# Kernel optimization log

Measured on AMD Instinct MI355X. Metric: run time of the kernel, lower is better.

Reference implementation:

```python
import jax, jax.numpy as jnp
import numpy as np

B, C, L = 2048, 9605, 8
ALPHA = 0.5        # self.alpha
ALPHA1 = 0.05      # margin
ALPHA2 = 2.0       # asymmetric scale when violated
ALPHA3 = 5.0       # logistic sharpness
ALPHA_OTHER = 0.3  # floor on top-k threshold
TOPK = 16          # x_sorted[15] -> 16th largest


def setup_inputs() -> dict:
    key = jax.random.key(0)
    k1, k2, k3, k4 = jax.random.split(key, 4)
    x = jax.random.normal(k1, (B, C), dtype=jnp.float32)
    # each class assigned to one of 5*L slots; slots < L are whitelist groups,
    # the rest are 'other' classes (like total_indices in the torch code)
    gid = jax.random.randint(k4, (C,), 0, 5 * L)
    gid = gid.at[:L].set(jnp.arange(L))  # guarantee every group is non-empty
    group_mask = gid[None, :] == jnp.arange(L)[:, None]  # [L, C] bool
    # sparse multi-label binarized targets (~14 positives/sample)
    y = (jax.random.uniform(k2, (B, C)) < 0.0015).astype(jnp.float32)
    y_neg = (jax.random.uniform(k3, (B, C)) < 0.0015).astype(jnp.float32)
    return {"x": x, "y": y, "y_neg": y_neg, "group_mask": group_mask}


def _rank_loss(x1, x2):
    # our_rank_loss: sigmoid(alpha3*(x2-x1+margin)), scaled by alpha2 when violated
    d = x2 - x1 + ALPHA1
    s = jax.nn.sigmoid(ALPHA3 * d)
    return jnp.where(d > 0, ALPHA2 * s, s)


def reference(x, y, y_neg, group_mask):
    xs = jax.nn.sigmoid(x)  # [B, C]
    # top_k_thres = max(16th-largest sigmoid score, alpha_other)
    thres = jnp.maximum(jax.lax.top_k(xs, TOPK)[0][:, TOPK - 1], ALPHA_OTHER)  # [B]
    maskf = group_mask.astype(xs.dtype)  # [L, C]
    neg_inf = jnp.array(-jnp.inf, xs.dtype)
    # per-sample max score inside each whitelist group: [B, L]
    group_max = jnp.max(jnp.where(group_mask[None, :, :], xs[:, None, :], neg_inf), axis=-1)
    # find_gt_whitelist: group is 'hit' if any positive target inside it
    gt = (y @ maskf.T) > 0        # [B, L]
    gt_neg = (y_neg @ maskf.T) > 0  # [B, L]
    has_gt = jnp.any(gt, axis=-1)    # [B]; False <=> sentinel len(all_labels)
    has_neg = jnp.any(gt_neg, axis=-1)
    # ---- case B: sample hits at least one whitelist group ----
    rl_correct = _rank_loss(group_max, thres[:, None])    # gt groups above thres
    rl_incorrect = _rank_loss(thres[:, None], group_max)  # non-gt groups below thres
    caseB = jnp.sum(jnp.where(gt, rl_correct, rl_incorrect), axis=-1)  # [B]
    # ---- case A: no whitelist group hit ----
    union = jnp.any(group_mask, axis=0)  # [C] union of all whitelist classes
    union_max = jnp.max(jnp.where(union[None, :], xs, neg_inf), axis=-1)  # [B]
    neg_max = jnp.max(jnp.where(gt_neg, group_max, neg_inf), axis=-1)
    neg_score = jnp.where(has_neg, neg_max, jnp.zeros((), xs.dtype))  # torch starts at 0
    caseA = (1.0 - ALPHA) * _rank_loss(thres, union_max) + ALPHA * _rank_loss(thres, neg_score)
    loss_rank_all = jnp.where(has_gt, caseB, caseA)  # [B]
    return jnp.mean(loss_rank_all)
```

## Files before the change

### kernel.cpp

```cpp
#include <hip/hip_runtime.h>
#include <math.h>

constexpr int B_ = 2048;
constexpr int C_ = 9605;
constexpr int L_ = 8;
constexpr int TOPK_ = 16;
constexpr int CAP_ = 512;
constexpr int NSLOT_ = 8;
constexpr float T0_ = 2.0f;
constexpr int QW_ = 2404;

__device__ __forceinline__ float sigm(float v) { return 1.0f / (1.0f + expf(-v)); }

__device__ __forceinline__ float rank_loss(float x1, float x2) {
  float d = x2 - x1 + 0.05f;
  float s = 1.0f / (1.0f + expf(-5.0f * d));
  return (d > 0.0f) ? 2.0f * s : s;
}

__device__ __forceinline__ unsigned int fkey(float v) {
  unsigned int u = __float_as_uint(v);
  return u ^ ((u & 0x80000000u) ? 0xFFFFFFFFu : 0x80000000u);
}
__device__ __forceinline__ float fkeyinv(unsigned int k) {
  unsigned int u = (k & 0x80000000u) ? (k ^ 0x80000000u) : ~k;
  return __uint_as_float(u);
}

__global__ void build_code_kernel(const int* __restrict__ mask,
                                  unsigned char* __restrict__ code) {
  int c = blockIdx.x * 256 + threadIdx.x;
  if (c >= C_) return;
  unsigned char cd = 0xFF;
#pragma unroll
  for (int l = L_ - 1; l >= 0; --l)
    if (mask[l * C_ + c] != 0) cd = (unsigned char)l;
  code[c] = cd;
}

__global__ void pack_code_kernel(const unsigned char* __restrict__ code,
                                 unsigned int* __restrict__ codeq) {
  int k = blockIdx.x * 256 + threadIdx.x;
  int r = blockIdx.y;
  if (k >= QW_) return;
  unsigned int v = 0u;
#pragma unroll
  for (int e = 0; e < 4; ++e) {
    int c = r + 4 * k + e;
    unsigned int byte = (c < C_) ? (unsigned int)code[c] : 0xFFu;
    v |= byte << (8 * e);
  }
  codeq[r * QW_ + k] = v;
}

__global__ void __launch_bounds__(256) row_loss_kernel(
    const float* __restrict__ x, const float* __restrict__ y,
    const float* __restrict__ yn, const unsigned char* __restrict__ code,
    const unsigned int* __restrict__ codeq, float* __restrict__ loss) {
  __shared__ float cand[CAP_];
  __shared__ int cand_cnt;
  __shared__ int s_of;
  __shared__ float wgm[4][L_];
  __shared__ unsigned int wgt[4], wgn[4];
  __shared__ float s_x16;
  __shared__ int s_red;

  const int t = threadIdx.x;
  const int b = blockIdx.x;
  const float* xr = x + (size_t)b * C_;
  const float* yr = y + (size_t)b * C_;
  const float* ynr = yn + (size_t)b * C_;

  if (t == 0) { cand_cnt = 0; s_of = 0; }

  float gm[L_];
#pragma unroll
  for (int l = 0; l < L_; ++l) gm[l] = -INFINITY;
  unsigned int gtb = 0u, gnb = 0u;
  float cnd[NSLOT_];
  int cc = 0;
#pragma unroll
  for (int k = 0; k < NSLOT_; ++k) cnd[k] = -INFINITY;

  auto proc = [&](float xv, float yv, float nv, int cd) {
#pragma unroll
    for (int l = 0; l < L_; ++l)
      if (cd == l) gm[l] = fmaxf(gm[l], xv);
    unsigned int mb = (cd < L_) ? (1u << (cd & 7)) : 0u;
    gtb |= (yv > 0.0f) ? mb : 0u;
    gnb |= (nv > 0.0f) ? mb : 0u;
    int cci = (xv > T0_) ? cc : NSLOT_;
#pragma unroll
    for (int k = 0; k < NSLOT_; ++k)
      if (cci == k) cnd[k] = xv;
    cc += (xv > T0_) ? 1 : 0;
  };

  const int r = b & 3;
  const int lead = (4 - r) & 3;
  const int n4 = (C_ - lead) >> 2;
  const float4* x4 = reinterpret_cast<const float4*>(x) + (((size_t)b * C_ + lead) >> 2);
  const float4* y4 = reinterpret_cast<const float4*>(y) + (((size_t)b * C_ + lead) >> 2);
  const float4* v4 = reinterpret_cast<const float4*>(yn) + (((size_t)b * C_ + lead) >> 2);
  const unsigned int* cq = codeq + lead * QW_;

  for (int k = t; k < n4; k += 256) {
    float4 xv = x4[k];
    float4 yv = y4[k];
    float4 nv = v4[k];
    unsigned int cqk = cq[k];
    proc(xv.x, yv.x, nv.x, (int)(cqk & 0xFF));
    proc(xv.y, yv.y, nv.y, (int)((cqk >> 8) & 0xFF));
    proc(xv.z, yv.z, nv.z, (int)((cqk >> 16) & 0xFF));
    proc(xv.w, yv.w, nv.w, (int)((cqk >> 24) & 0xFF));
  }
  if (t < lead) proc(xr[t], yr[t], ynr[t], (int)code[t]);
  const int tstart = lead + (n4 << 2);
  if (t >= 4 && t < 4 + (C_ - tstart)) {
    int c = tstart + (t - 4);
    proc(xr[c], yr[c], ynr[c], (int)code[c]);
  }

#pragma unroll
  for (int off = 32; off > 0; off >>= 1) {
#pragma unroll
    for (int l = 0; l < L_; ++l) gm[l] = fmaxf(gm[l], __shfl_xor(gm[l], off, 64));
    gtb |= (unsigned int)__shfl_xor((int)gtb, off, 64);
    gnb |= (unsigned int)__shfl_xor((int)gnb, off, 64);
  }

  __syncthreads();

  int nw = (cc < NSLOT_) ? cc : NSLOT_;
  if (nw > 0) {
    int pos = atomicAdd(&cand_cnt, nw);
#pragma unroll
    for (int k = 0; k < NSLOT_; ++k)
      if (k < nw && pos + k < CAP_) cand[pos + k] = cnd[k];
  }
  if (cc > NSLOT_) atomicOr(&s_of, 1);

  if ((t & 63) == 0) {
    int w = t >> 6;
#pragma unroll
    for (int l = 0; l < L_; ++l) wgm[w][l] = gm[l];
    wgt[w] = gtb;
    wgn[w] = gnb;
  }
  __syncthreads();

  const int cnt = cand_cnt;
  const bool mainp = (cnt >= TOPK_) && (cnt <= CAP_) && (s_of == 0);
  if (mainp) {
    if (t < 64) {
      unsigned int ku[CAP_ / 64];
#pragma unroll
      for (int k = 0; k < CAP_ / 64; ++k) {
        int idx = t + (k << 6);
        ku[k] = (idx < cnt) ? fkey(cand[idx]) : 0u;
      }
      unsigned int lo = 0u, hi = 0xFFFFFFFFu;
      for (int it = 0; it < 32 && lo < hi; ++it) {
        unsigned int mid = lo + ((hi - lo) >> 1) + 1u;
        int c16 = 0;
#pragma unroll
        for (int k = 0; k < CAP_ / 64; ++k) c16 += (ku[k] >= mid) ? 1 : 0;
#pragma unroll
        for (int off = 32; off > 0; off >>= 1) c16 += __shfl_xor(c16, off, 64);
        if (c16 >= TOPK_) lo = mid; else hi = mid - 1u;
      }
      if (t == 0) s_x16 = fkeyinv(lo);
    }
  } else {
    unsigned int lo = 0u, hi = 0xFFFFFFFFu;
    for (int it = 0; it < 32; ++it) {
      if (lo >= hi) break;
      unsigned int mid = lo + ((hi - lo) >> 1) + 1u;
      if (t == 0) s_red = 0;
      __syncthreads();
      int cl = 0;
      for (int c = t; c < C_; c += 256) cl += (fkey(xr[c]) >= mid) ? 1 : 0;
      atomicAdd(&s_red, cl);
      __syncthreads();
      int total = s_red;
      __syncthreads();
      if (total >= TOPK_) lo = mid; else hi = mid - 1u;
    }
    if (t == 0) s_x16 = fkeyinv(lo);
  }
  __syncthreads();

  if (t == 0) {
    float thres = fmaxf(sigm(s_x16), 0.3f);
    unsigned int gtbf = wgt[0] | wgt[1] | wgt[2] | wgt[3];
    unsigned int gnbf = wgn[0] | wgn[1] | wgn[2] | wgn[3];
    float caseB = 0.0f, unio = -INFINITY, negmax = -INFINITY;
#pragma unroll
    for (int l = 0; l < L_; ++l) {
      float gx = fmaxf(fmaxf(wgm[0][l], wgm[1][l]), fmaxf(wgm[2][l], wgm[3][l]));
      float g = sigm(gx);
      unio = fmaxf(unio, g);
      caseB += ((gtbf >> l) & 1u) ? rank_loss(g, thres) : rank_loss(thres, g);
      if ((gnbf >> l) & 1u) negmax = fmaxf(negmax, g);
    }
    float negscore = (gnbf != 0u) ? negmax : 0.0f;
    float caseA = 0.5f * rank_loss(thres, unio) + 0.5f * rank_loss(thres, negscore);
    loss[b] = (gtbf != 0u) ? caseB : caseA;
  }
}

__global__ void mean_kernel(const float* __restrict__ loss, float* __restrict__ out) {
  const int t = threadIdx.x;
  float s = 0.0f;
  for (int i = t; i < B_; i += 256) s += loss[i];
#pragma unroll
  for (int off = 32; off > 0; off >>= 1) s += __shfl_xor(s, off, 64);
  __shared__ float part[4];
  if ((t & 63) == 0) part[t >> 6] = s;
  __syncthreads();
  if (t == 0) out[0] = (part[0] + part[1] + part[2] + part[3]) * (1.0f / (float)B_);
}

extern "C" void kernel_launch(void* const* d_in, const int* in_sizes, int n_in,
                              void* d_out, int out_size, void* d_ws, size_t ws_size,
                              hipStream_t stream) {
  const float* x = (const float*)d_in[0];
  const float* y = (const float*)d_in[1];
  const float* yn = (const float*)d_in[2];
  const int* mask = (const int*)d_in[3];

  float* loss = (float*)d_ws;
  unsigned char* code = (unsigned char*)d_ws + 8192;
  unsigned int* codeq = (unsigned int*)((char*)d_ws + 8192 + 9612);

  hipLaunchKernelGGL(build_code_kernel, dim3((C_ + 255) / 256), dim3(256), 0, stream,
                     mask, code);
  hipLaunchKernelGGL(pack_code_kernel, dim3((QW_ + 255) / 256, 4), dim3(256), 0, stream,
                     code, codeq);
  hipLaunchKernelGGL(row_loss_kernel, dim3(B_), dim3(256), 0, stream,
                     x, y, yn, code, codeq, loss);
  hipLaunchKernelGGL(mean_kernel, dim3(1), dim3(256), 0, stream,
                     loss, (float*)d_out);
}
```

Before: 262.0 us.

## Split sparse target scanning into separate grid-wide kernel with atomic group bits

Moves the scan of y and y_neg out of the per-row kernel into a dedicated grid-stride kernel that streams both arrays and atomically ORs group bits only for rare positive entries. The row kernel now reads just x and the packed codes, with unrolled float4 loads and a direct shared-memory atomic append for candidates in place of per-thread slot registers. The aim is to cut per-row work and register pressure and raise memory parallelism. The cost is an extra memset, an extra kernel launch and global atomics, and total traffic over y and y_neg is unchanged.

New measurement: 262.1 us. Within noise of the previous version (+0.0%).

```diff
diff --git a/kernel.cpp b/kernel.cpp
--- a/kernel.cpp
+++ b/kernel.cpp
@@ -6,9 +6,9 @@
 constexpr int L_ = 8;
 constexpr int TOPK_ = 16;
 constexpr int CAP_ = 512;
-constexpr int NSLOT_ = 8;
 constexpr float T0_ = 2.0f;
 constexpr int QW_ = 2404;
+constexpr int NQ_ = (B_ * C_) / 4;
 
 __device__ __forceinline__ float sigm(float v) { return 1.0f / (1.0f + expf(-v)); }
 
@@ -53,104 +53,132 @@
   codeq[r * QW_ + k] = v;
 }
 
+__global__ void __launch_bounds__(256) scan_pos_kernel(
+    const float* __restrict__ y, const float* __restrict__ yn,
+    const unsigned char* __restrict__ code,
+    unsigned int* __restrict__ gtb, unsigned int* __restrict__ gnb) {
+  const float* arr = (blockIdx.y == 0) ? y : yn;
+  unsigned int* dst = (blockIdx.y == 0) ? gtb : gnb;
+  const float4* a4 = reinterpret_cast<const float4*>(arr);
+  const int S = gridDim.x * 256;
+  int q = blockIdx.x * 256 + threadIdx.x;
+
+  auto rare = [&](float v, int idx) {
+    if (v > 0.0f) {
+      int row = idx / C_;
+      int col = idx - row * C_;
+      unsigned char cd = code[col];
+      if (cd < L_) atomicOr(&dst[row], 1u << cd);
+    }
+  };
+  auto chk = [&](float4 v, int qq) {
+    float m = fmaxf(fmaxf(v.x, v.y), fmaxf(v.z, v.w));
+    if (m > 0.0f) {
+      int base = qq << 2;
+      rare(v.x, base); rare(v.y, base + 1); rare(v.z, base + 2); rare(v.w, base + 3);
+    }
+  };
+
+  for (; q + 3 * S < NQ_; q += 4 * S) {
+    float4 v0 = a4[q];
+    float4 v1 = a4[q + S];
+    float4 v2 = a4[q + 2 * S];
+    float4 v3 = a4[q + 3 * S];
+    chk(v0, q); chk(v1, q + S); chk(v2, q + 2 * S); chk(v3, q + 3 * S);
+  }
+  for (; q < NQ_; q += S) chk(a4[q], q);
+}
+
 __global__ void __launch_bounds__(256) row_loss_kernel(
-    const float* __restrict__ x, const float* __restrict__ y,
-    const float* __restrict__ yn, const unsigned char* __restrict__ code,
-    const unsigned int* __restrict__ codeq, float* __restrict__ loss) {
+    const float* __restrict__ x, const unsigned char* __restrict__ code,
+    const unsigned int* __restrict__ codeq,
+    const unsigned int* __restrict__ gtb_g, const unsigned int* __restrict__ gnb_g,
+    float* __restrict__ loss) {
   __shared__ float cand[CAP_];
   __shared__ int cand_cnt;
-  __shared__ int s_of;
   __shared__ float wgm[4][L_];
-  __shared__ unsigned int wgt[4], wgn[4];
   __shared__ float s_x16;
   __shared__ int s_red;
 
   const int t = threadIdx.x;
   const int b = blockIdx.x;
   const float* xr = x + (size_t)b * C_;
-  const float* yr = y + (size_t)b * C_;
-  const float* ynr = yn + (size_t)b * C_;
-
-  if (t == 0) { cand_cnt = 0; s_of = 0; }
+  if (t == 0) cand_cnt = 0;
 
   float gm[L_];
 #pragma unroll
   for (int l = 0; l < L_; ++l) gm[l] = -INFINITY;
-  unsigned int gtb = 0u, gnb = 0u;
-  float cnd[NSLOT_];
-  int cc = 0;
-#pragma unroll
-  for (int k = 0; k < NSLOT_; ++k) cnd[k] = -INFINITY;
-
-  auto proc = [&](float xv, float yv, float nv, int cd) {
-#pragma unroll
-    for (int l = 0; l < L_; ++l)
-      if (cd == l) gm[l] = fmaxf(gm[l], xv);
-    unsigned int mb = (cd < L_) ? (1u << (cd & 7)) : 0u;
-    gtb |= (yv > 0.0f) ? mb : 0u;
-    gnb |= (nv > 0.0f) ? mb : 0u;
-    int cci = (xv > T0_) ? cc : NSLOT_;
-#pragma unroll
-    for (int k = 0; k < NSLOT_; ++k)
-      if (cci == k) cnd[k] = xv;
-    cc += (xv > T0_) ? 1 : 0;
-  };
-
-  const int r = b & 3;
-  const int lead = (4 - r) & 3;
+
+  auto cappend = [&](float xv) {
+    int p = atomicAdd(&cand_cnt, 1);
+    if (p < CAP_) cand[p] = xv;
+  };
+  auto procq = [&](float4 xv, unsigned int cd4) {
+    int c0 = (int)(cd4 & 0xFF), c1 = (int)((cd4 >> 8) & 0xFF);
+    int c2 = (int)((cd4 >> 16) & 0xFF), c3 = (int)((cd4 >> 24) & 0xFF);
+#pragma unroll
+    for (int l = 0; l < L_; ++l) {
+      float vl = (c0 == l) ? xv.x : -INFINITY;
+      vl = (c1 == l) ? fmaxf(vl, xv.y) : vl;
+      vl = (c2 == l) ? fmaxf(vl, xv.z) : vl;
+      vl = (c3 == l) ? fmaxf(vl, xv.w) : vl;
+      gm[l] = fmaxf(gm[l], vl);
+    }
+    if (xv.x > T0_) cappend(xv.x);
+    if (xv.y > T0_) cappend(xv.y);
+    if (xv.z > T0_) cappend(xv.z);
+    if (xv.w > T0_) cappend(xv.w);
+  };
+
+  const int lead = (4 - (b & 3)) & 3;
   const int n4 = (C_ - lead) >> 2;
   const float4* x4 = reinterpret_cast<const float4*>(x) + (((size_t)b * C_ + lead) >> 2);
-  const float4* y4 = reinterpret_cast<const float4*>(y) + (((size_t)b * C_ + lead) >> 2);
-  const float4* v4 = reinterpret_cast<const float4*>(yn) + (((size_t)b * C_ + lead) >> 2);
   const unsigned int* cq = codeq + lead * QW_;
 
-  for (int k = t; k < n4; k += 256) {
-    float4 xv = x4[k];
-    float4 yv = y4[k];
-    float4 nv = v4[k];
-    unsigned int cqk = cq[k];
-    proc(xv.x, yv.x, nv.x, (int)(cqk & 0xFF));
-    proc(xv.y, yv.y, nv.y, (int)((cqk >> 8) & 0xFF));
-    proc(xv.z, yv.z, nv.z, (int)((cqk >> 16) & 0xFF));
-    proc(xv.w, yv.w, nv.w, (int)((cqk >> 24) & 0xFF));
-  }
-  if (t < lead) proc(xr[t], yr[t], ynr[t], (int)code[t]);
+  for (int kb = 0; kb < 2048; kb += 1024) {
+    int k0 = kb + t, k1 = kb + 256 + t, k2 = kb + 512 + t, k3 = kb + 768 + t;
+    float4 a0 = x4[k0];
+    float4 a1 = x4[k1];
+    float4 a2 = x4[k2];
+    float4 a3 = x4[k3];
+    unsigned int q0 = cq[k0], q1 = cq[k1], q2 = cq[k2], q3 = cq[k3];
+    procq(a0, q0); procq(a1, q1); procq(a2, q2); procq(a3, q3);
+  }
+  for (int k = 2048 + t; k < n4; k += 256) procq(x4[k], cq[k]);
+
+  if (t < lead) {
+    float v = xr[t];
+    int cd = (int)code[t];
+#pragma unroll
+    for (int l = 0; l < L_; ++l)
+      if (cd == l) gm[l] = fmaxf(gm[l], v);
+    if (v > T0_) cappend(v);
+  }
   const int tstart = lead + (n4 << 2);
   if (t >= 4 && t < 4 + (C_ - tstart)) {
     int c = tstart + (t - 4);
-    proc(xr[c], yr[c], ynr[c], (int)code[c]);
+    float v = xr[c];
+    int cd = (int)code[c];
+#pragma unroll
+    for (int l = 0; l < L_; ++l)
+      if (cd == l) gm[l] = fmaxf(gm[l], v);
+    if (v > T0_) cappend(v);
   }
 
 #pragma unroll
   for (int off = 32; off > 0; off >>= 1) {
 #pragma unroll
     for (int l = 0; l < L_; ++l) gm[l] = fmaxf(gm[l], __shfl_xor(gm[l], off, 64));
-    gtb |= (unsigned int)__shfl_xor((int)gtb, off, 64);
-    gnb |= (unsigned int)__shfl_xor((int)gnb, off, 64);
-  }
-
-  __syncthreads();
-
-  int nw = (cc < NSLOT_) ? cc : NSLOT_;
-  if (nw > 0) {
-    int pos = atomicAdd(&cand_cnt, nw);
-#pragma unroll
-    for (int k = 0; k < NSLOT_; ++k)
-      if (k < nw && pos + k < CAP_) cand[pos + k] = cnd[k];
-  }
-  if (cc > NSLOT_) atomicOr(&s_of, 1);
-
+  }
   if ((t & 63) == 0) {
     int w = t >> 6;
 #pragma unroll
     for (int l = 0; l < L_; ++l) wgm[w][l] = gm[l];
-    wgt[w] = gtb;
-    wgn[w] = gnb;
   }
   __syncthreads();
 
   const int cnt = cand_cnt;
-  const bool mainp = (cnt >= TOPK_) && (cnt <= CAP_) && (s_of == 0);
+  const bool mainp = (cnt >= TOPK_) && (cnt <= CAP_);
   if (mainp) {
     if (t < 64) {
       unsigned int ku[CAP_ / 64];
@@ -192,8 +220,8 @@
 
   if (t == 0) {
     float thres = fmaxf(sigm(s_x16), 0.3f);
-    unsigned int gtbf = wgt[0] | wgt[1] | wgt[2] | wgt[3];
-    unsigned int gnbf = wgn[0] | wgn[1] | wgn[2] | wgn[3];
+    unsigned int gtbf = gtb_g[b];
+    unsigned int gnbf = gnb_g[b];
     float caseB = 0.0f, unio = -INFINITY, negmax = -INFINITY;
 #pragma unroll
     for (int l = 0; l < L_; ++l) {
@@ -229,16 +257,22 @@
   const float* yn = (const float*)d_in[2];
   const int* mask = (const int*)d_in[3];
 
-  float* loss = (float*)d_ws;
-  unsigned char* code = (unsigned char*)d_ws + 8192;
-  unsigned int* codeq = (unsigned int*)((char*)d_ws + 8192 + 9612);
-
+  char* ws = (char*)d_ws;
+  float* loss = (float*)ws;
+  unsigned int* gtb = (unsigned int*)(ws + 8192);
+  unsigned int* gnb = (unsigned int*)(ws + 16384);
+  unsigned char* code = (unsigned char*)(ws + 24576);
+  unsigned int* codeq = (unsigned int*)(ws + 24576 + 9632);
+
+  hipMemsetAsync(gtb, 0, 2 * B_ * sizeof(unsigned int), stream);
   hipLaunchKernelGGL(build_code_kernel, dim3((C_ + 255) / 256), dim3(256), 0, stream,
                      mask, code);
   hipLaunchKernelGGL(pack_code_kernel, dim3((QW_ + 255) / 256, 4), dim3(256), 0, stream,
                      code, codeq);
+  hipLaunchKernelGGL(scan_pos_kernel, dim3(2048, 2), dim3(256), 0, stream,
+                     y, yn, code, gtb, gnb);
   hipLaunchKernelGGL(row_loss_kernel, dim3(B_), dim3(256), 0, stream,
-                     x, y, yn, code, codeq, loss);
+                     x, code, codeq, gtb, gnb, loss);
   hipLaunchKernelGGL(mean_kernel, dim3(1), dim3(256), 0, stream,
                      loss, (float*)d_out);
 }
```
